# Kernel tuning notes

Hardware: AMD Instinct MI355X
Metric: run time of the kernel (lower is better)

Reference implementation:

```python
import jax, jax.numpy as jnp
import numpy as np

N_ATOM = 2048
C_ATOM = 128
C_PAIR = 16
N_HEADS = 4
BLOCK = 128
EPS = 1e-5


def _layernorm(x):
    mu = jnp.mean(x, axis=-1, keepdims=True)
    var = jnp.mean(jnp.square(x - mu), axis=-1, keepdims=True)
    return (x - mu) / jnp.sqrt(var + EPS)


def setup_inputs() -> dict:
    key = jax.random.key(0)
    ks = jax.random.split(key, 12)
    s = 0.02
    x = jax.random.normal(ks[0], (N_ATOM, C_ATOM), jnp.float32)
    pair_emb = jax.random.normal(ks[1], (N_ATOM, N_ATOM, C_PAIR), jnp.float32)
    block_index = jax.random.randint(ks[2], (N_ATOM, BLOCK), 0, N_ATOM, jnp.int64)
    Wq = jax.random.normal(ks[3], (C_ATOM, C_ATOM), jnp.float32) * s
    Wk = jax.random.normal(ks[4], (C_ATOM, C_ATOM), jnp.float32) * s
    Wv = jax.random.normal(ks[5], (C_ATOM, C_ATOM), jnp.float32) * s
    Wb = jax.random.normal(ks[6], (N_HEADS, 1), jnp.float32) * s  # nn.Linear(1, num_heads)
    Wout = jax.random.normal(ks[7], (C_ATOM, C_ATOM), jnp.float32) * s
    W1 = jax.random.normal(ks[8], (4 * C_ATOM, C_ATOM), jnp.float32) * s
    b1 = jnp.zeros((4 * C_ATOM,), jnp.float32)
    W2 = jax.random.normal(ks[9], (C_ATOM, 4 * C_ATOM), jnp.float32) * s
    b2 = jnp.zeros((C_ATOM,), jnp.float32)
    return {"x": x, "pair_emb": pair_emb, "block_index": block_index,
            "Wq": Wq, "Wk": Wk, "Wv": Wv, "Wb": Wb, "Wout": Wout,
            "W1": W1, "b1": b1, "W2": W2, "b2": b2}


def reference(x, pair_emb, block_index, Wq, Wk, Wv, Wb, Wout, W1, b1, W2, b2):
    N = x.shape[0]
    d_head = C_ATOM // N_HEADS
    h = _layernorm(x)
    q = (h @ Wq.T).reshape(N, N_HEADS, d_head)
    k = (h @ Wk.T).reshape(N, N_HEADS, d_head)
    v = (h @ Wv.T).reshape(N, N_HEADS, d_head)

    # pair bias per head: mean over c_pair, then Linear(1 -> n_heads)
    pair_mean = jnp.mean(pair_emb, axis=-1)              # [N, N]
    pair_bias = pair_mean[..., None] * Wb[:, 0]          # [N, N, H]

    # local block-sparse attention: each query i attends to keys block_index[i]
    k_g = k[block_index]                                 # [N, B, H, d]
    v_g = v[block_index]                                 # [N, B, H, d]
    rows = jnp.arange(N)[:, None]
    bias = pair_bias[rows, block_index]                  # [N, B, H]

    scale = 1.0 / jnp.sqrt(jnp.asarray(d_head, q.dtype))
    scores = jnp.einsum('nhd,nbhd->nhb', q, k_g) * scale + jnp.transpose(bias, (0, 2, 1))
    attn = jax.nn.softmax(scores, axis=-1)               # [N, H, B]
    attn_out = jnp.einsum('nhb,nbhd->nhd', attn, v_g).reshape(N, C_ATOM)

    x = x + attn_out @ Wout.T
    h2 = _layernorm(x)
    mlp = jax.nn.silu(h2 @ W1.T + b1) @ W2.T + b2
    return x + mlp
```

## Files before the change

kernel.cpp:

```cpp
#include <hip/hip_runtime.h>
#include <hip/hip_bf16.h>

#define N_ATOMS 2048
#define C_DIM   128
#define C_PAIR  16
#define BLK_K   128
#define LN_EPS  1e-5f

typedef float f32x4 __attribute__((ext_vector_type(4)));
typedef short s16x8 __attribute__((ext_vector_type(8)));

__device__ __forceinline__ float bf_lo(unsigned int p) {
    union { unsigned int i; float f; } u; u.i = p << 16; return u.f;
}
__device__ __forceinline__ float bf_hi(unsigned int p) {
    union { unsigned int i; float f; } u; u.i = p & 0xffff0000u; return u.f;
}
__device__ __forceinline__ float bf2f(unsigned short s) {
    union { unsigned int i; float f; } u; u.i = ((unsigned int)s) << 16; return u.f;
}
__device__ __forceinline__ unsigned short f2bf(float f) {
    union { float f; unsigned int i; } u; u.f = f;
    const unsigned int r = u.i + 0x7fffu + ((u.i >> 16) & 1u);
    return (unsigned short)(r >> 16);
}

__device__ __forceinline__ s16x8 lda_frag(const unsigned short* base,
                                          int rowBytes, int kstep, int lane) {
    const int m    = lane & 15;
    const int koff = kstep * 64 + ((lane >> 4) << 4);
    const int addr = m * rowBytes + (koff ^ ((m & 7) << 4));
    return *reinterpret_cast<const s16x8*>(
        reinterpret_cast<const char*>(base) + addr);
}

__device__ void pack_unit(int u, int lane,
                          const float* __restrict__ Wout,
                          const float* __restrict__ W1,
                          const float* __restrict__ W2,
                          unsigned short* __restrict__ WoutP,
                          unsigned short* __restrict__ W1P,
                          unsigned short* __restrict__ W2P)
{
    const float* W; unsigned short* P; int K, local;
    if (u < 32)       { W = Wout; P = WoutP; K = 128; local = u; }
    else if (u < 160) { W = W1;   P = W1P;   K = 128; local = u - 32; }
    else              { W = W2;   P = W2P;   K = 512; local = u - 160; }
    const int ksteps = K >> 5;
    const int ntile  = local / ksteps;
    const int kstep  = local - ntile * ksteps;
    const int n  = ntile * 16 + (lane & 15);
    const int k0 = kstep * 32 + ((lane >> 4) << 3);
    const float4* src = reinterpret_cast<const float4*>(W + (size_t)n * K + k0);
    const float4 a = src[0], b = src[1];
    s16x8 o;
    o[0] = (short)f2bf(a.x); o[1] = (short)f2bf(a.y);
    o[2] = (short)f2bf(a.z); o[3] = (short)f2bf(a.w);
    o[4] = (short)f2bf(b.x); o[5] = (short)f2bf(b.y);
    o[6] = (short)f2bf(b.z); o[7] = (short)f2bf(b.w);
    reinterpret_cast<s16x8*>(P)[local * 64 + lane] = o;
}

__global__ __launch_bounds__(512) void ln_qkv_kernel(
    const float* __restrict__ x,
    const float* __restrict__ Wq, const float* __restrict__ Wk,
    const float* __restrict__ Wv,
    const float* __restrict__ Wout, const float* __restrict__ W1,
    const float* __restrict__ W2,
    float* __restrict__ q,
    unsigned short* __restrict__ kb, unsigned short* __restrict__ vb,
    unsigned short* __restrict__ WoutP, unsigned short* __restrict__ W1P,
    unsigned short* __restrict__ W2P)
{
    __shared__ __align__(16) unsigned short hB[16][128];
    const int t = threadIdx.x;
    const int bid = blockIdx.x;
    const int row0 = bid * 16;

    if (t < 64)       pack_unit(bid * 2,     t,       Wout, W1, W2, WoutP, W1P, W2P);
    else if (t < 128) pack_unit(bid * 2 + 1, t - 64,  Wout, W1, W2, WoutP, W1P, W2P);
    else if (t < 192 && bid < 32)
                      pack_unit(256 + bid,   t - 128, Wout, W1, W2, WoutP, W1P, W2P);

    {
        const int r = t >> 5, l = t & 31;
        const float4 xv = reinterpret_cast<const float4*>(
            x + (size_t)(row0 + r) * C_DIM)[l];
        float s  = xv.x + xv.y + xv.z + xv.w;
        float ss = xv.x*xv.x + xv.y*xv.y + xv.z*xv.z + xv.w*xv.w;
        #pragma unroll
        for (int m = 16; m >= 1; m >>= 1) {
            s  += __shfl_xor(s,  m);
            ss += __shfl_xor(ss, m);
        }
        const float mu  = s * (1.0f / 128.0f);
        const float var = ss * (1.0f / 128.0f) - mu * mu;
        const float inv = rsqrtf(var + LN_EPS);
        union { unsigned long long u64; unsigned short u16[4]; } pk;
        pk.u16[0] = f2bf((xv.x - mu) * inv);
        pk.u16[1] = f2bf((xv.y - mu) * inv);
        pk.u16[2] = f2bf((xv.z - mu) * inv);
        pk.u16[3] = f2bf((xv.w - mu) * inv);
        *reinterpret_cast<unsigned long long*>(
            reinterpret_cast<char*>(&hB[0][0]) +
            r * 256 + ((l * 8) ^ ((r & 7) << 4))) = pk.u64;
    }
    __syncthreads();

    {
        const int wv = t >> 6, lane = t & 63;
        s16x8 afr[4];
        #pragma unroll
        for (int ks = 0; ks < 4; ++ks) afr[ks] = lda_frag(&hB[0][0], 256, ks, lane);

        const int n = wv * 16 + (lane & 15);
        #pragma unroll
        for (int p = 0; p < 3; ++p) {
            const float* W = (p == 0) ? Wq : (p == 1) ? Wk : Wv;
            f32x4 acc = {0.f, 0.f, 0.f, 0.f};
            #pragma unroll
            for (int ks = 0; ks < 4; ++ks) {
                const int k0 = ks * 32 + ((lane >> 4) << 3);
                const float4* src = reinterpret_cast<const float4*>(
                    W + (size_t)n * C_DIM + k0);
                const float4 a = src[0], b = src[1];
                s16x8 bfr;
                bfr[0] = (short)f2bf(a.x); bfr[1] = (short)f2bf(a.y);
                bfr[2] = (short)f2bf(a.z); bfr[3] = (short)f2bf(a.w);
                bfr[4] = (short)f2bf(b.x); bfr[5] = (short)f2bf(b.y);
                bfr[6] = (short)f2bf(b.z); bfr[7] = (short)f2bf(b.w);
                acc = __builtin_amdgcn_mfma_f32_16x16x32_bf16(afr[ks], bfr, acc, 0, 0, 0);
            }
            #pragma unroll
            for (int ii = 0; ii < 4; ++ii) {
                const int m = ((lane >> 4) << 2) + ii;
                const size_t off = (size_t)(row0 + m) * C_DIM + n;
                if (p == 0)      q[off]  = acc[ii];
                else if (p == 1) kb[off] = f2bf(acc[ii]);
                else             vb[off] = f2bf(acc[ii]);
            }
        }
    }
}

__global__ __launch_bounds__(1024) void attn_mlp_kernel(
    const float* __restrict__ q, const unsigned short* __restrict__ kb,
    const unsigned short* __restrict__ vb, const float* __restrict__ pair,
    const int*  __restrict__ bidx, const float* __restrict__ Wb,
    const float* __restrict__ x,
    const unsigned short* __restrict__ WoutP,
    const unsigned short* __restrict__ W1P, const float* __restrict__ b1,
    const unsigned short* __restrict__ W2P, const float* __restrict__ b2,
    float* __restrict__ out)
{
    __shared__ __align__(16) float qS[8][128];
    __shared__ __align__(16) int   idxS[8][128];
    __shared__ __align__(16) float S[8][4][128];
    __shared__ __align__(16) float ys[8][128];
    __shared__ __align__(16) unsigned short aoB[16][128];
    __shared__ __align__(16) unsigned short h2B[16][128];
    __shared__ __align__(16) unsigned short gsB[16][512];

    const int t = threadIdx.x;
    const int row0 = blockIdx.x * 8;
    const int r = t >> 7;
    const int u = t & 127;
    const int row = row0 + r;
    const int wv = t >> 6, lane = t & 63;

    const int j = bidx[(size_t)row * BLK_K + u];
    idxS[r][u] = j;
    qS[r][u] = q[(size_t)row * C_DIM + u];
    if (t < 256) {
        const int r2 = t >> 5, l = t & 31;
        const float4 xv = reinterpret_cast<const float4*>(
            x + (size_t)(row0 + r2) * C_DIM)[l];
        *reinterpret_cast<float4*>(&ys[r2][l * 4]) = xv;
    } else if (t < 384) {
        const uint4 z = {0,0,0,0};
        reinterpret_cast<uint4*>(&aoB[8][0])[t - 256] = z;
    } else if (t < 512) {
        const uint4 z = {0,0,0,0};
        reinterpret_cast<uint4*>(&h2B[8][0])[t - 384] = z;
    } else {
        const uint4 z = {0,0,0,0};
        reinterpret_cast<uint4*>(&gsB[8][0])[t - 512] = z;
    }
    const f32x4* pr = reinterpret_cast<const f32x4*>(
        pair + ((size_t)row * N_ATOMS + (size_t)j) * C_PAIR);
    const f32x4 p0 = __builtin_nontemporal_load(pr + 0);
    const f32x4 p1 = __builtin_nontemporal_load(pr + 1);
    const f32x4 p2 = __builtin_nontemporal_load(pr + 2);
    const f32x4 p3 = __builtin_nontemporal_load(pr + 3);
    __syncthreads();

    {
        const uint4* kr = reinterpret_cast<const uint4*>(kb + (size_t)j * C_DIM);
        const float4* q4 = reinterpret_cast<const float4*>(&qS[r][0]);
        float sc[4];
        #pragma unroll
        for (int h = 0; h < 4; ++h) {
            float a = 0.f;
            #pragma unroll
            for (int d = 0; d < 4; ++d) {
                const uint4  kk = kr[h * 4 + d];
                const float4 qa = q4[h * 8 + d * 2];
                const float4 qc = q4[h * 8 + d * 2 + 1];
                a += bf_lo(kk.x)*qa.x + bf_hi(kk.x)*qa.y
                   + bf_lo(kk.y)*qa.z + bf_hi(kk.y)*qa.w;
                a += bf_lo(kk.z)*qc.x + bf_hi(kk.z)*qc.y
                   + bf_lo(kk.w)*qc.z + bf_hi(kk.w)*qc.w;
            }
            sc[h] = a;
        }
        const float pm = (p0.x+p0.y+p0.z+p0.w + p1.x+p1.y+p1.z+p1.w +
                          p2.x+p2.y+p2.z+p2.w + p3.x+p3.y+p3.z+p3.w) * (1.0f/16.0f);
        const float scale = 0.17677669529663687f;
        #pragma unroll
        for (int h = 0; h < 4; ++h)
            S[r][h][u] = sc[h] * scale + pm * Wb[h];
    }
    __syncthreads();

    {
        const int g = u >> 5, l = u & 31;
        const float v0 = S[r][g][l],      v1 = S[r][g][l + 32],
                    v2 = S[r][g][l + 64], v3 = S[r][g][l + 96];
        float mx = fmaxf(fmaxf(v0, v1), fmaxf(v2, v3));
        #pragma unroll
        for (int m = 16; m >= 1; m >>= 1) mx = fmaxf(mx, __shfl_xor(mx, m));
        const float e0 = __expf(v0 - mx), e1 = __expf(v1 - mx),
                    e2 = __expf(v2 - mx), e3 = __expf(v3 - mx);
        float sm = e0 + e1 + e2 + e3;
        #pragma unroll
        for (int m = 16; m >= 1; m >>= 1) sm += __shfl_xor(sm, m);
        const float rs = 1.0f / sm;
        S[r][g][l]      = e0 * rs;
        S[r][g][l + 32] = e1 * rs;
        S[r][g][l + 64] = e2 * rs;
        S[r][g][l + 96] = e3 * rs;
    }
    __syncthreads();

    {
        const int hh = u >> 5;
        const float4* Sv = reinterpret_cast<const float4*>(&S[r][hh][0]);
        const int4*   iv = reinterpret_cast<const int4*>(&idxS[r][0]);
        float acc = 0.f;
        #pragma unroll 8
        for (int bq = 0; bq < 32; ++bq) {
            const float4 s4 = Sv[bq];
            const int4   j4 = iv[bq];
            acc += s4.x * bf2f(vb[(size_t)j4.x * C_DIM + u]);
            acc += s4.y * bf2f(vb[(size_t)j4.y * C_DIM + u]);
            acc += s4.z * bf2f(vb[(size_t)j4.z * C_DIM + u]);
            acc += s4.w * bf2f(vb[(size_t)j4.w * C_DIM + u]);
        }
        *reinterpret_cast<unsigned short*>(
            reinterpret_cast<char*>(&aoB[0][0]) +
            r * 256 + (((u * 2)) ^ ((r & 7) << 4))) = f2bf(acc);
    }
    __syncthreads();

    if (wv < 8) {
        f32x4 acc = {0.f, 0.f, 0.f, 0.f};
        const s16x8* Bp = reinterpret_cast<const s16x8*>(WoutP);
        #pragma unroll
        for (int ks = 0; ks < 4; ++ks) {
            const s16x8 a = lda_frag(&aoB[0][0], 256, ks, lane);
            const s16x8 b = Bp[(wv * 4 + ks) * 64 + lane];
            acc = __builtin_amdgcn_mfma_f32_16x16x32_bf16(a, b, acc, 0, 0, 0);
        }
        if (lane < 32) {
            const int c = wv * 16 + (lane & 15);
            #pragma unroll
            for (int i = 0; i < 4; ++i) {
                const int m = ((lane >> 4) << 2) + i;
                ys[m][c] += acc[i];
            }
        }
    }
    __syncthreads();

    if (t < 256) {
        const int rr = t >> 5, l = t & 31;
        const float4 yv = *reinterpret_cast<const float4*>(&ys[rr][l * 4]);
        float s  = yv.x + yv.y + yv.z + yv.w;
        float ss = yv.x*yv.x + yv.y*yv.y + yv.z*yv.z + yv.w*yv.w;
        #pragma unroll
        for (int m = 16; m >= 1; m >>= 1) {
            s  += __shfl_xor(s,  m);
            ss += __shfl_xor(ss, m);
        }
        const float mu  = s * (1.0f / 128.0f);
        const float var = ss * (1.0f / 128.0f) - mu * mu;
        const float inv = rsqrtf(var + LN_EPS);
        union { unsigned long long u64; unsigned short u16[4]; } pk;
        pk.u16[0] = f2bf((yv.x - mu) * inv);
        pk.u16[1] = f2bf((yv.y - mu) * inv);
        pk.u16[2] = f2bf((yv.z - mu) * inv);
        pk.u16[3] = f2bf((yv.w - mu) * inv);
        *reinterpret_cast<unsigned long long*>(
            reinterpret_cast<char*>(&h2B[0][0]) +
            rr * 256 + ((l * 8) ^ ((rr & 7) << 4))) = pk.u64;
    }
    __syncthreads();

    {
        s16x8 afr[4];
        #pragma unroll
        for (int ks = 0; ks < 4; ++ks) afr[ks] = lda_frag(&h2B[0][0], 256, ks, lane);
        const s16x8* Bp = reinterpret_cast<const s16x8*>(W1P);
        #pragma unroll
        for (int tt = 0; tt < 2; ++tt) {
            const int tile = wv * 2 + tt;
            f32x4 acc = {0.f, 0.f, 0.f, 0.f};
            #pragma unroll
            for (int ks = 0; ks < 4; ++ks) {
                const s16x8 b = Bp[(tile * 4 + ks) * 64 + lane];
                acc = __builtin_amdgcn_mfma_f32_16x16x32_bf16(afr[ks], b, acc, 0, 0, 0);
            }
            if (lane < 32) {
                const int c = tile * 16 + (lane & 15);
                const float bb = b1[c];
                #pragma unroll
                for (int i = 0; i < 4; ++i) {
                    const int m = ((lane >> 4) << 2) + i;
                    const float g = acc[i] + bb;
                    const float sv = g / (1.0f + __expf(-g));
                    *reinterpret_cast<unsigned short*>(
                        reinterpret_cast<char*>(&gsB[0][0]) +
                        m * 1024 + ((c * 2) ^ ((m & 7) << 4))) = f2bf(sv);
                }
            }
        }
    }
    __syncthreads();

    if (wv < 8) {
        f32x4 acc = {0.f, 0.f, 0.f, 0.f};
        const s16x8* Bp = reinterpret_cast<const s16x8*>(W2P);
        #pragma unroll
        for (int ks = 0; ks < 16; ++ks) {
            const s16x8 a = lda_frag(&gsB[0][0], 1024, ks, lane);
            const s16x8 b = Bp[(wv * 16 + ks) * 64 + lane];
            acc = __builtin_amdgcn_mfma_f32_16x16x32_bf16(a, b, acc, 0, 0, 0);
        }
        if (lane < 32) {
            const int c = wv * 16 + (lane & 15);
            const float bb = b2[c];
            #pragma unroll
            for (int i = 0; i < 4; ++i) {
                const int m = ((lane >> 4) << 2) + i;
                out[(size_t)(row0 + m) * C_DIM + c] = ys[m][c] + bb + acc[i];
            }
        }
    }
}

extern "C" void kernel_launch(void* const* d_in, const int* in_sizes, int n_in,
                              void* d_out, int out_size, void* d_ws, size_t ws_size,
                              hipStream_t stream)
{
    const float* x    = (const float*)d_in[0];
    const float* pair = (const float*)d_in[1];
    const int*   bidx = (const int*)  d_in[2];
    const float* Wq   = (const float*)d_in[3];
    const float* Wk   = (const float*)d_in[4];
    const float* Wv   = (const float*)d_in[5];
    const float* Wb   = (const float*)d_in[6];
    const float* Wout = (const float*)d_in[7];
    const float* W1   = (const float*)d_in[8];
    const float* b1   = (const float*)d_in[9];
    const float* W2   = (const float*)d_in[10];
    const float* b2   = (const float*)d_in[11];
    float* out = (float*)d_out;

    char* ws = (char*)d_ws;
    float*          q     = (float*)ws;
    unsigned short* kb    = (unsigned short*)(ws + (1 << 20));
    unsigned short* vb    = (unsigned short*)(ws + (1 << 20) + (1 << 19));
    unsigned short* WoutP = (unsigned short*)(ws + (2 << 20));
    unsigned short* W1P   = (unsigned short*)(ws + (2 << 20) + (32 << 10));
    unsigned short* W2P   = (unsigned short*)(ws + (2 << 20) + (160 << 10));

    hipLaunchKernelGGL(ln_qkv_kernel, dim3(N_ATOMS / 16), dim3(512), 0, stream,
                       x, Wq, Wk, Wv, Wout, W1, W2, q, kb, vb, WoutP, W1P, W2P);
    hipLaunchKernelGGL(attn_mlp_kernel, dim3(N_ATOMS / 8), dim3(1024), 0, stream,
                       q, kb, vb, pair, bidx, Wb, x, WoutP, W1P, b1, W2P, b2, out);
}
```

Before: 42.76 us.

## Restructure attention kernel to one wave per row with in-wave softmax

```diff
diff --git a/kernel.cpp b/kernel.cpp
--- a/kernel.cpp
+++ b/kernel.cpp
@@ -15,9 +15,6 @@
 }
 __device__ __forceinline__ float bf_hi(unsigned int p) {
     union { unsigned int i; float f; } u; u.i = p & 0xffff0000u; return u.f;
-}
-__device__ __forceinline__ float bf2f(unsigned short s) {
-    union { unsigned int i; float f; } u; u.i = ((unsigned int)s) << 16; return u.f;
 }
 __device__ __forceinline__ unsigned short f2bf(float f) {
     union { float f; unsigned int i; } u; u.f = f;
@@ -143,7 +140,7 @@
     }
 }
 
-__global__ __launch_bounds__(1024) void attn_mlp_kernel(
+__global__ __launch_bounds__(512, 4) void attn_mlp_kernel(
     const float* __restrict__ q, const unsigned short* __restrict__ kb,
     const unsigned short* __restrict__ vb, const float* __restrict__ pair,
     const int*  __restrict__ bidx, const float* __restrict__ Wb,
@@ -155,7 +152,7 @@
 {
     __shared__ __align__(16) float qS[8][128];
     __shared__ __align__(16) int   idxS[8][128];
-    __shared__ __align__(16) float S[8][4][128];
+    __shared__ __align__(16) float Sl[8][4][128];
     __shared__ __align__(16) float ys[8][128];
     __shared__ __align__(16) unsigned short aoB[16][128];
     __shared__ __align__(16) unsigned short h2B[16][128];
@@ -163,121 +160,137 @@
 
     const int t = threadIdx.x;
     const int row0 = blockIdx.x * 8;
-    const int r = t >> 7;
-    const int u = t & 127;
-    const int row = row0 + r;
-    const int wv = t >> 6, lane = t & 63;
-
-    const int j = bidx[(size_t)row * BLK_K + u];
-    idxS[r][u] = j;
-    qS[r][u] = q[(size_t)row * C_DIM + u];
-    if (t < 256) {
-        const int r2 = t >> 5, l = t & 31;
-        const float4 xv = reinterpret_cast<const float4*>(
-            x + (size_t)(row0 + r2) * C_DIM)[l];
-        *reinterpret_cast<float4*>(&ys[r2][l * 4]) = xv;
-    } else if (t < 384) {
+    const int w = t >> 6, lane = t & 63;
+    const int row = row0 + w;
+
+    {
         const uint4 z = {0,0,0,0};
-        reinterpret_cast<uint4*>(&aoB[8][0])[t - 256] = z;
-    } else if (t < 512) {
-        const uint4 z = {0,0,0,0};
-        reinterpret_cast<uint4*>(&h2B[8][0])[t - 384] = z;
-    } else {
-        const uint4 z = {0,0,0,0};
-        reinterpret_cast<uint4*>(&gsB[8][0])[t - 512] = z;
-    }
-    const f32x4* pr = reinterpret_cast<const f32x4*>(
-        pair + ((size_t)row * N_ATOMS + (size_t)j) * C_PAIR);
-    const f32x4 p0 = __builtin_nontemporal_load(pr + 0);
-    const f32x4 p1 = __builtin_nontemporal_load(pr + 1);
-    const f32x4 p2 = __builtin_nontemporal_load(pr + 2);
-    const f32x4 p3 = __builtin_nontemporal_load(pr + 3);
+        if (t < 128)      reinterpret_cast<uint4*>(&aoB[8][0])[t] = z;
+        else if (t < 256) reinterpret_cast<uint4*>(&h2B[8][0])[t - 128] = z;
+        reinterpret_cast<uint4*>(&gsB[8][0])[t] = z;
+        if (t < 256) {
+            const int r2 = t >> 5, l2 = t & 31;
+            const float4 xv = reinterpret_cast<const float4*>(
+                x + (size_t)(row0 + r2) * C_DIM)[l2];
+            *reinterpret_cast<float4*>(&ys[r2][l2 * 4]) = xv;
+        }
+    }
+
+    const int j0 = bidx[(size_t)row * BLK_K + lane];
+    const int j1 = bidx[(size_t)row * BLK_K + 64 + lane];
+    idxS[w][lane] = j0;
+    idxS[w][64 + lane] = j1;
+    {
+        const float2 q2 = *reinterpret_cast<const float2*>(
+            q + (size_t)row * C_DIM + 2 * lane);
+        *reinterpret_cast<float2*>(&qS[w][2 * lane]) = q2;
+    }
+
+    const f32x4* pr0 = reinterpret_cast<const f32x4*>(
+        pair + ((size_t)row * N_ATOMS + (size_t)j0) * C_PAIR);
+    const f32x4* pr1 = reinterpret_cast<const f32x4*>(
+        pair + ((size_t)row * N_ATOMS + (size_t)j1) * C_PAIR);
+    const f32x4 pa0 = __builtin_nontemporal_load(pr0 + 0);
+    const f32x4 pa1 = __builtin_nontemporal_load(pr0 + 1);
+    const f32x4 pa2 = __builtin_nontemporal_load(pr0 + 2);
+    const f32x4 pa3 = __builtin_nontemporal_load(pr0 + 3);
+    const f32x4 pb0 = __builtin_nontemporal_load(pr1 + 0);
+    const f32x4 pb1 = __builtin_nontemporal_load(pr1 + 1);
+    const f32x4 pb2 = __builtin_nontemporal_load(pr1 + 2);
+    const f32x4 pb3 = __builtin_nontemporal_load(pr1 + 3);
+
+    float sc0[4], sc1[4];
+    {
+        const uint4* kr0 = reinterpret_cast<const uint4*>(kb + (size_t)j0 * C_DIM);
+        const uint4* kr1 = reinterpret_cast<const uint4*>(kb + (size_t)j1 * C_DIM);
+        #pragma unroll
+        for (int h = 0; h < 4; ++h) {
+            float a0 = 0.f, a1 = 0.f;
+            #pragma unroll
+            for (int c = 0; c < 4; ++c) {
+                const uint4 k0 = kr0[h * 4 + c];
+                const uint4 k1 = kr1[h * 4 + c];
+                const float4 qa = *reinterpret_cast<const float4*>(
+                    &qS[w][h * 32 + c * 8]);
+                const float4 qc = *reinterpret_cast<const float4*>(
+                    &qS[w][h * 32 + c * 8 + 4]);
+                a0 += bf_lo(k0.x)*qa.x + bf_hi(k0.x)*qa.y
+                    + bf_lo(k0.y)*qa.z + bf_hi(k0.y)*qa.w
+                    + bf_lo(k0.z)*qc.x + bf_hi(k0.z)*qc.y
+                    + bf_lo(k0.w)*qc.z + bf_hi(k0.w)*qc.w;
+                a1 += bf_lo(k1.x)*qa.x + bf_hi(k1.x)*qa.y
+                    + bf_lo(k1.y)*qa.z + bf_hi(k1.y)*qa.w
+                    + bf_lo(k1.z)*qc.x + bf_hi(k1.z)*qc.y
+                    + bf_lo(k1.w)*qc.z + bf_hi(k1.w)*qc.w;
+            }
+            sc0[h] = a0; sc1[h] = a1;
+        }
+    }
+
+    const float pm0 = (pa0.x+pa0.y+pa0.z+pa0.w + pa1.x+pa1.y+pa1.z+pa1.w +
+                       pa2.x+pa2.y+pa2.z+pa2.w + pa3.x+pa3.y+pa3.z+pa3.w) * (1.0f/16.0f);
+    const float pm1 = (pb0.x+pb0.y+pb0.z+pb0.w + pb1.x+pb1.y+pb1.z+pb1.w +
+                       pb2.x+pb2.y+pb2.z+pb2.w + pb3.x+pb3.y+pb3.z+pb3.w) * (1.0f/16.0f);
+    const float scale = 0.17677669529663687f;
+
+    #pragma unroll
+    for (int h = 0; h < 4; ++h) {
+        const float wb = Wb[h];
+        const float s0 = sc0[h] * scale + pm0 * wb;
+        const float s1 = sc1[h] * scale + pm1 * wb;
+        float mx = fmaxf(s0, s1);
+        #pragma unroll
+        for (int m = 32; m >= 1; m >>= 1) mx = fmaxf(mx, __shfl_xor(mx, m));
+        const float e0 = __expf(s0 - mx), e1 = __expf(s1 - mx);
+        float sm = e0 + e1;
+        #pragma unroll
+        for (int m = 32; m >= 1; m >>= 1) sm += __shfl_xor(sm, m);
+        const float rs = 1.0f / sm;
+        Sl[w][h][lane]      = e0 * rs;
+        Sl[w][h][lane + 64] = e1 * rs;
+    }
+
+    {
+        const int d0 = 2 * lane;
+        const int hh = lane >> 4;
+        float acc0 = 0.f, acc1 = 0.f;
+        #pragma unroll 8
+        for (int k4 = 0; k4 < 32; ++k4) {
+            const int4   j4 = *reinterpret_cast<const int4*>(&idxS[w][k4 * 4]);
+            const float4 p4 = *reinterpret_cast<const float4*>(&Sl[w][hh][k4 * 4]);
+            unsigned int v01;
+            v01 = *reinterpret_cast<const unsigned int*>(vb + (size_t)j4.x * C_DIM + d0);
+            acc0 += p4.x * bf_lo(v01); acc1 += p4.x * bf_hi(v01);
+            v01 = *reinterpret_cast<const unsigned int*>(vb + (size_t)j4.y * C_DIM + d0);
+            acc0 += p4.y * bf_lo(v01); acc1 += p4.y * bf_hi(v01);
+            v01 = *reinterpret_cast<const unsigned int*>(vb + (size_t)j4.z * C_DIM + d0);
+            acc0 += p4.z * bf_lo(v01); acc1 += p4.z * bf_hi(v01);
+            v01 = *reinterpret_cast<const unsigned int*>(vb + (size_t)j4.w * C_DIM + d0);
+            acc0 += p4.w * bf_lo(v01); acc1 += p4.w * bf_hi(v01);
+        }
+        const unsigned int pk = (unsigned int)f2bf(acc0) |
+                                ((unsigned int)f2bf(acc1) << 16);
+        *reinterpret_cast<unsigned int*>(
+            reinterpret_cast<char*>(&aoB[0][0]) +
+            w * 256 + ((4 * lane) ^ ((w & 7) << 4))) = pk;
+    }
+
     __syncthreads();
 
     {
-        const uint4* kr = reinterpret_cast<const uint4*>(kb + (size_t)j * C_DIM);
-        const float4* q4 = reinterpret_cast<const float4*>(&qS[r][0]);
-        float sc[4];
-        #pragma unroll
-        for (int h = 0; h < 4; ++h) {
-            float a = 0.f;
-            #pragma unroll
-            for (int d = 0; d < 4; ++d) {
-                const uint4  kk = kr[h * 4 + d];
-                const float4 qa = q4[h * 8 + d * 2];
-                const float4 qc = q4[h * 8 + d * 2 + 1];
-                a += bf_lo(kk.x)*qa.x + bf_hi(kk.x)*qa.y
-                   + bf_lo(kk.y)*qa.z + bf_hi(kk.y)*qa.w;
-                a += bf_lo(kk.z)*qc.x + bf_hi(kk.z)*qc.y
-                   + bf_lo(kk.w)*qc.z + bf_hi(kk.w)*qc.w;
-            }
-            sc[h] = a;
-        }
-        const float pm = (p0.x+p0.y+p0.z+p0.w + p1.x+p1.y+p1.z+p1.w +
-                          p2.x+p2.y+p2.z+p2.w + p3.x+p3.y+p3.z+p3.w) * (1.0f/16.0f);
-        const float scale = 0.17677669529663687f;
-        #pragma unroll
-        for (int h = 0; h < 4; ++h)
-            S[r][h][u] = sc[h] * scale + pm * Wb[h];
-    }
-    __syncthreads();
-
-    {
-        const int g = u >> 5, l = u & 31;
-        const float v0 = S[r][g][l],      v1 = S[r][g][l + 32],
-                    v2 = S[r][g][l + 64], v3 = S[r][g][l + 96];
-        float mx = fmaxf(fmaxf(v0, v1), fmaxf(v2, v3));
-        #pragma unroll
-        for (int m = 16; m >= 1; m >>= 1) mx = fmaxf(mx, __shfl_xor(mx, m));
-        const float e0 = __expf(v0 - mx), e1 = __expf(v1 - mx),
-                    e2 = __expf(v2 - mx), e3 = __expf(v3 - mx);
-        float sm = e0 + e1 + e2 + e3;
-        #pragma unroll
-        for (int m = 16; m >= 1; m >>= 1) sm += __shfl_xor(sm, m);
-        const float rs = 1.0f / sm;
-        S[r][g][l]      = e0 * rs;
-        S[r][g][l + 32] = e1 * rs;
-        S[r][g][l + 64] = e2 * rs;
-        S[r][g][l + 96] = e3 * rs;
-    }
-    __syncthreads();
-
-    {
-        const int hh = u >> 5;
-        const float4* Sv = reinterpret_cast<const float4*>(&S[r][hh][0]);
-        const int4*   iv = reinterpret_cast<const int4*>(&idxS[r][0]);
-        float acc = 0.f;
-        #pragma unroll 8
-        for (int bq = 0; bq < 32; ++bq) {
-            const float4 s4 = Sv[bq];
-            const int4   j4 = iv[bq];
-            acc += s4.x * bf2f(vb[(size_t)j4.x * C_DIM + u]);
-            acc += s4.y * bf2f(vb[(size_t)j4.y * C_DIM + u]);
-            acc += s4.z * bf2f(vb[(size_t)j4.z * C_DIM + u]);
-            acc += s4.w * bf2f(vb[(size_t)j4.w * C_DIM + u]);
-        }
-        *reinterpret_cast<unsigned short*>(
-            reinterpret_cast<char*>(&aoB[0][0]) +
-            r * 256 + (((u * 2)) ^ ((r & 7) << 4))) = f2bf(acc);
-    }
-    __syncthreads();
-
-    if (wv < 8) {
         f32x4 acc = {0.f, 0.f, 0.f, 0.f};
         const s16x8* Bp = reinterpret_cast<const s16x8*>(WoutP);
         #pragma unroll
         for (int ks = 0; ks < 4; ++ks) {
             const s16x8 a = lda_frag(&aoB[0][0], 256, ks, lane);
-            const s16x8 b = Bp[(wv * 4 + ks) * 64 + lane];
+            const s16x8 b = Bp[(w * 4 + ks) * 64 + lane];
             acc = __builtin_amdgcn_mfma_f32_16x16x32_bf16(a, b, acc, 0, 0, 0);
         }
-        if (lane < 32) {
-            const int c = wv * 16 + (lane & 15);
-            #pragma unroll
-            for (int i = 0; i < 4; ++i) {
-                const int m = ((lane >> 4) << 2) + i;
-                ys[m][c] += acc[i];
-            }
+        const int c = w * 16 + (lane & 15);
+        #pragma unroll
+        for (int i = 0; i < 4; ++i) {
+            const int m = ((lane >> 4) << 2) + i;
+            if (m < 8) ys[m][c] += acc[i];
         }
     }
     __syncthreads();
@@ -312,20 +325,20 @@
         for (int ks = 0; ks < 4; ++ks) afr[ks] = lda_frag(&h2B[0][0], 256, ks, lane);
         const s16x8* Bp = reinterpret_cast<const s16x8*>(W1P);
         #pragma unroll
-        for (int tt = 0; tt < 2; ++tt) {
-            const int tile = wv * 2 + tt;
+        for (int tt = 0; tt < 4; ++tt) {
+            const int tile = w * 4 + tt;
             f32x4 acc = {0.f, 0.f, 0.f, 0.f};
             #pragma unroll
             for (int ks = 0; ks < 4; ++ks) {
                 const s16x8 b = Bp[(tile * 4 + ks) * 64 + lane];
                 acc = __builtin_amdgcn_mfma_f32_16x16x32_bf16(afr[ks], b, acc, 0, 0, 0);
             }
-            if (lane < 32) {
-                const int c = tile * 16 + (lane & 15);
-                const float bb = b1[c];
-                #pragma unroll
-                for (int i = 0; i < 4; ++i) {
-                    const int m = ((lane >> 4) << 2) + i;
+            const int c = tile * 16 + (lane & 15);
+            const float bb = b1[c];
+            #pragma unroll
+            for (int i = 0; i < 4; ++i) {
+                const int m = ((lane >> 4) << 2) + i;
+                if (m < 8) {
                     const float g = acc[i] + bb;
                     const float sv = g / (1.0f + __expf(-g));
                     *reinterpret_cast<unsigned short*>(
@@ -337,23 +350,22 @@
     }
     __syncthreads();
 
-    if (wv < 8) {
+    {
         f32x4 acc = {0.f, 0.f, 0.f, 0.f};
         const s16x8* Bp = reinterpret_cast<const s16x8*>(W2P);
         #pragma unroll
         for (int ks = 0; ks < 16; ++ks) {
             const s16x8 a = lda_frag(&gsB[0][0], 1024, ks, lane);
-            const s16x8 b = Bp[(wv * 16 + ks) * 64 + lane];
+            const s16x8 b = Bp[(w * 16 + ks) * 64 + lane];
             acc = __builtin_amdgcn_mfma_f32_16x16x32_bf16(a, b, acc, 0, 0, 0);
         }
-        if (lane < 32) {
-            const int c = wv * 16 + (lane & 15);
-            const float bb = b2[c];
-            #pragma unroll
-            for (int i = 0; i < 4; ++i) {
-                const int m = ((lane >> 4) << 2) + i;
+        const int c = w * 16 + (lane & 15);
+        const float bb = b2[c];
+        #pragma unroll
+        for (int i = 0; i < 4; ++i) {
+            const int m = ((lane >> 4) << 2) + i;
+            if (m < 8)
                 out[(size_t)(row0 + m) * C_DIM + c] = ys[m][c] + bb + acc[i];
-            }
         }
     }
 }
@@ -386,6 +398,6 @@
 
     hipLaunchKernelGGL(ln_qkv_kernel, dim3(N_ATOMS / 16), dim3(512), 0, stream,
                        x, Wq, Wk, Wv, Wout, W1, W2, q, kb, vb, WoutP, W1P, W2P);
-    hipLaunchKernelGGL(attn_mlp_kernel, dim3(N_ATOMS / 8), dim3(1024), 0, stream,
+    hipLaunchKernelGGL(attn_mlp_kernel, dim3(N_ATOMS / 8), dim3(512), 0, stream,
                        q, kb, vb, pair, bidx, Wb, x, WoutP, W1P, b1, W2P, b2, out);
 }
```

Result: slower. 44.88 us (+5.0%).
